# Performance work log

Hardware: AMD Instinct MI355X
Metric: run time of the kernel (lower is better)

Reference implementation:

```python
import jax, jax.numpy as jnp
import numpy as np

N_NODES = 100000


def gcn_conv(x, W, b, src, dst, n):
    # x: [N, Fin], W: [Fin, Fout]. GCNConv: D^-1/2 (A+I) D^-1/2 (X W) + b
    h = x @ W  # [N, Fout]
    ones = jnp.ones_like(dst, dtype=h.dtype)
    deg = jax.ops.segment_sum(ones, dst, num_segments=n)  # in-degree incl self-loops
    dinv = jnp.where(deg > 0, jax.lax.rsqrt(deg), 0.0)
    norm = dinv[src] * dinv[dst]  # [E]
    msg = h[src] * norm[:, None]  # gather + scale
    out = jax.ops.segment_sum(msg, dst, num_segments=n)  # scatter-add
    return out + b


def setup_inputs() -> dict:
    key = jax.random.key(0)
    k1, k2, k3, k4 = jax.random.split(key, 4)
    F_IN, H, C, E = 512, 256, 40, 3200000
    x = jax.random.normal(k1, (N_NODES, F_IN), dtype=jnp.float32)
    # glorot-ish init
    W1 = jax.random.normal(k2, (F_IN, H), dtype=jnp.float32) * (1.0 / np.sqrt(F_IN))
    b1 = jnp.zeros((H,), dtype=jnp.float32)
    W2 = jax.random.normal(k3, (H, C), dtype=jnp.float32) * (1.0 / np.sqrt(H))
    b2 = jnp.zeros((C,), dtype=jnp.float32)
    edge_index = jax.random.randint(k4, (2, E), 0, N_NODES, dtype=jnp.int64)
    return {"x": x, "W1": W1, "b1": b1, "W2": W2, "b2": b2, "edge_index": edge_index}


def reference(x, W1, b1, W2, b2, edge_index):
    n = x.shape[0]
    # add self-loops (PyG GCNConv default add_self_loops=True)
    loop = jnp.arange(n, dtype=edge_index.dtype)
    src = jnp.concatenate([edge_index[0], loop])
    dst = jnp.concatenate([edge_index[1], loop])
    h = gcn_conv(x, W1, b1, src, dst, n)
    h = jax.nn.relu(h)
    # F.dropout(training=self.training): identity in eval mode
    h = gcn_conv(h, W2, b2, src, dst, n)
    return jax.nn.log_softmax(h, axis=1)
```

## Files before the change

kernel.cpp:

```cpp
#include <hip/hip_runtime.h>
#include <stdint.h>

typedef __attribute__((ext_vector_type(8))) short bf16x8;
typedef __attribute__((ext_vector_type(4))) float f32x4;
typedef __attribute__((ext_vector_type(4))) int i32x4;
typedef __attribute__((ext_vector_type(2))) float f32x2;
typedef __attribute__((ext_vector_type(4))) unsigned int u32x4;
typedef __attribute__((ext_vector_type(8))) unsigned short ushort8_t;

__device__ __forceinline__ unsigned short f2bf(float f) {
    unsigned int u = __float_as_uint(f);
    u += 0x7FFFu + ((u >> 16) & 1u);
    return (unsigned short)(u >> 16);
}
__device__ __forceinline__ float bf2f(unsigned short s) {
    return __uint_as_float(((unsigned int)s) << 16);
}
__device__ __forceinline__ unsigned char fp8_enc(float f) {
    f = fminf(fmaxf(f, -448.f), 448.f);
    unsigned int u = __float_as_uint(f * 0x1p-120f);
    u += 0x7FFFFu + ((u >> 20) & 1u);
    return (unsigned char)(((u >> 20) & 0x7F) | ((u >> 24) & 0x80));
}

__device__ __forceinline__ f32x2 cvtpk0(unsigned int u) {
#if __has_builtin(__builtin_amdgcn_cvt_pk_f32_fp8)
    auto r = __builtin_amdgcn_cvt_pk_f32_fp8((int)u, false);
    f32x2 o; o.x = r[0]; o.y = r[1]; return o;
#else
    f32x2 o;
    o.x = __builtin_amdgcn_cvt_f32_fp8(u, 0);
    o.y = __builtin_amdgcn_cvt_f32_fp8(u, 1);
    return o;
#endif
}
__device__ __forceinline__ f32x2 cvtpk1(unsigned int u) {
#if __has_builtin(__builtin_amdgcn_cvt_pk_f32_fp8)
    auto r = __builtin_amdgcn_cvt_pk_f32_fp8((int)u, true);
    f32x2 o; o.x = r[0]; o.y = r[1]; return o;
#else
    f32x2 o;
    o.x = __builtin_amdgcn_cvt_f32_fp8(u, 2);
    o.y = __builtin_amdgcn_cvt_f32_fp8(u, 3);
    return o;
#endif
}

#define SLAB_CAP 5120

__global__ __launch_bounds__(256) void k_bscatter(const int* __restrict__ src,
                                                  const int* __restrict__ dst, int E,
                                                  int* __restrict__ bcnt,
                                                  int* __restrict__ slab, int nbuck) {
    __shared__ int lh[1024];
    __shared__ int lcur[1024];
    const int CH = 8192;
    int e0 = blockIdx.x * CH;
    int e1 = min(E, e0 + CH);
    for (int i = threadIdx.x; i < nbuck; i += 256) lh[i] = 0;
    __syncthreads();
    for (int i = e0 + threadIdx.x; i < e1; i += 256) atomicAdd(&lh[dst[i] >> 7], 1);
    __syncthreads();
    for (int i = threadIdx.x; i < nbuck; i += 256) {
        int c = lh[i];
        lh[i] = c ? atomicAdd(&bcnt[i], c) : 0;
        lcur[i] = 0;
    }
    __syncthreads();
    for (int i = e0 + threadIdx.x; i < e1; i += 256) {
        int d = dst[i], s = src[i];
        int b = d >> 7;
        int p = lh[b] + atomicAdd(&lcur[b], 1);
        if (p < SLAB_CAP) slab[(size_t)b * SLAB_CAP + p] = ((d & 127) << 20) | s;
    }
}

__global__ __launch_bounds__(1024) void k_bscan(const int* __restrict__ bcnt,
                                                int* __restrict__ bbase, int nbuck) {
    __shared__ int sh[1024];
    int t = threadIdx.x;
    int v = (t < nbuck) ? min(bcnt[t], SLAB_CAP) : 0;
    sh[t] = v;
    __syncthreads();
    for (int off = 1; off < 1024; off <<= 1) {
        int x = (t >= off) ? sh[t - off] : 0;
        __syncthreads();
        sh[t] += x;
        __syncthreads();
    }
    if (t < nbuck) bbase[t] = sh[t] - v;
    if (t == 1023) bbase[nbuck] = sh[1023];
}

__global__ __launch_bounds__(256) void k_bcsr(const int* __restrict__ slab,
                                              const int* __restrict__ bcnt,
                                              const int* __restrict__ bbase,
                                              int* __restrict__ rowp,
                                              int* __restrict__ col,
                                              float* __restrict__ dinv, int n, int nbuck) {
    __shared__ int lh[128], lsc[128], lcur[128];
    const int b = blockIdx.x;
    const int base = bbase[b];
    const int cnt = min(bcnt[b], SLAB_CAP);
    const int t = threadIdx.x;
    const int* sl = slab + (size_t)b * SLAB_CAP;
    if (t < 128) lh[t] = 0;
    __syncthreads();
    for (int i = t; i < cnt; i += 256) atomicAdd(&lh[sl[i] >> 20], 1);
    __syncthreads();
    if (t < 128) lsc[t] = lh[t];
    __syncthreads();
    for (int off = 1; off < 128; off <<= 1) {
        int x = (t < 128 && t >= off) ? lsc[t - off] : 0;
        __syncthreads();
        if (t < 128) lsc[t] += x;
        __syncthreads();
    }
    if (t < 128) {
        int excl = lsc[t] - lh[t];
        lcur[t] = excl;
        int v = (b << 7) + t;
        if (v < n) {
            rowp[v] = base + excl;
            dinv[v] = rsqrtf((float)lh[t] + 1.0f);
        }
    }
    if (b == 0 && t == 0) rowp[n] = bbase[nbuck];
    __syncthreads();
    for (int i = t; i < cnt; i += 256) {
        int pk = sl[i];
        int d = pk >> 20;
        int p = base + atomicAdd(&lcur[d], 1);
        col[p] = pk & 0xFFFFF;
    }
}

__global__ __launch_bounds__(256) void k_cvt_w(const float* __restrict__ W1,
                                               const float* __restrict__ W2,
                                               short* __restrict__ W1t,
                                               short* __restrict__ W2t,
                                               int n1, int n2) {
    int i = blockIdx.x * blockDim.x + threadIdx.x;
    if (i < n1) {
        int k = i >> 8, c = i & 255;
        W1t[(size_t)c * 512 + k] = (short)f2bf(W1[i]);
    } else if (i < n1 + n2) {
        int i2 = i - n1;
        int k = i2 / 40, c = i2 - k * 40;
        W2t[(size_t)c * 256 + k] = (short)f2bf(W2[i2]);
    }
}

__global__ __launch_bounds__(512) void k_gemm1(const float* __restrict__ A,
                                               const short* __restrict__ Bt,
                                               const float* __restrict__ dinv,
                                               unsigned char* __restrict__ outp, int M) {
    const int K = 512;
    __shared__ __align__(16) short As[128 * 32];
    __shared__ __align__(16) short Bs[256 * 32];
    const int tid = threadIdx.x;
    const int m0 = blockIdx.x * 128;
    const int w = tid >> 6, lane = tid & 63;
    const int quad = lane >> 4, l16 = lane & 15;
    const int mbase = (w >> 2) * 64, nbase = (w & 3) * 64;

    f32x4 acc[4][4];
#pragma unroll
    for (int i = 0; i < 4; i++)
#pragma unroll
        for (int j = 0; j < 4; j++) acc[i][j] = (f32x4){0.f, 0.f, 0.f, 0.f};

    for (int k0 = 0; k0 < K; k0 += 32) {
#pragma unroll
        for (int s = tid; s < 1024; s += 512) {
            int r = s >> 3, seg = s & 7;
            int gr = m0 + r;
            if (gr >= M) gr = M - 1;
            float4 v = *(const float4*)(A + (size_t)gr * K + k0 + seg * 4);
            ushort4 o;
            o.x = f2bf(v.x); o.y = f2bf(v.y); o.z = f2bf(v.z); o.w = f2bf(v.w);
            *(ushort4*)(As + r * 32 + seg * 4) = o;
        }
#pragma unroll
        for (int s = tid; s < 1024; s += 512) {
            int r = s >> 2, seg = s & 3;
            i32x4 v = *(const i32x4*)(Bt + (size_t)r * K + k0 + seg * 8);
            *(i32x4*)(Bs + r * 32 + seg * 8) = v;
        }
        __syncthreads();
        bf16x8 af[4], bfr[4];
#pragma unroll
        for (int i = 0; i < 4; i++)
            af[i] = *(const bf16x8*)(As + (mbase + i * 16 + l16) * 32 + quad * 8);
#pragma unroll
        for (int j = 0; j < 4; j++)
            bfr[j] = *(const bf16x8*)(Bs + (nbase + j * 16 + l16) * 32 + quad * 8);
#pragma unroll
        for (int i = 0; i < 4; i++)
#pragma unroll
            for (int j = 0; j < 4; j++)
                acc[i][j] = __builtin_amdgcn_mfma_f32_16x16x32_bf16(af[i], bfr[j], acc[i][j], 0, 0, 0);
        __syncthreads();
    }

#pragma unroll
    for (int i = 0; i < 4; i++) {
#pragma unroll
        for (int r = 0; r < 4; r++) {
            int row = m0 + mbase + i * 16 + quad * 4 + r;
            if (row < M) {
                float dv = dinv[row] * 64.f;
#pragma unroll
                for (int j = 0; j < 4; j++)
                    outp[(size_t)row * 256 + nbase + j * 16 + l16] =
                        fp8_enc(acc[i][j][r] * dv);
            }
        }
    }
}

__global__ __launch_bounds__(256) void k_gemm2(const short* __restrict__ A,
                                               const short* __restrict__ Bt,
                                               const float* __restrict__ dinv,
                                               unsigned char* __restrict__ outp, int M) {
    const int K = 256;
    __shared__ __align__(16) short As[128 * 32];
    __shared__ __align__(16) short Bs[64 * 32];
    const int tid = threadIdx.x;
    const int m0 = blockIdx.x * 128;
    const int w = tid >> 6, lane = tid & 63;
    const int quad = lane >> 4, l16 = lane & 15;
    const int mbase = (w >> 1) * 64, nbase = (w & 1) * 32;

    f32x4 acc[4][2];
#pragma unroll
    for (int i = 0; i < 4; i++)
#pragma unroll
        for (int j = 0; j < 2; j++) acc[i][j] = (f32x4){0.f, 0.f, 0.f, 0.f};

    for (int k0 = 0; k0 < K; k0 += 32) {
#pragma unroll
        for (int s = tid; s < 512; s += 256) {
            int r = s >> 2, seg = s & 3;
            int gr = m0 + r;
            if (gr >= M) gr = M - 1;
            i32x4 v = *(const i32x4*)(A + (size_t)gr * K + k0 + seg * 8);
            *(i32x4*)(As + r * 32 + seg * 8) = v;
        }
        if (tid < 256) {
            int r = tid >> 2, seg = tid & 3;
            i32x4 v = *(const i32x4*)(Bt + (size_t)r * K + k0 + seg * 8);
            *(i32x4*)(Bs + r * 32 + seg * 8) = v;
        }
        __syncthreads();
        bf16x8 af[4], bfr[2];
#pragma unroll
        for (int i = 0; i < 4; i++)
            af[i] = *(const bf16x8*)(As + (mbase + i * 16 + l16) * 32 + quad * 8);
#pragma unroll
        for (int j = 0; j < 2; j++)
            bfr[j] = *(const bf16x8*)(Bs + (nbase + j * 16 + l16) * 32 + quad * 8);
#pragma unroll
        for (int i = 0; i < 4; i++)
#pragma unroll
            for (int j = 0; j < 2; j++)
                acc[i][j] = __builtin_amdgcn_mfma_f32_16x16x32_bf16(af[i], bfr[j], acc[i][j], 0, 0, 0);
        __syncthreads();
    }

#pragma unroll
    for (int i = 0; i < 4; i++) {
#pragma unroll
        for (int r = 0; r < 4; r++) {
            int row = m0 + mbase + i * 16 + quad * 4 + r;
            if (row < M) {
                float dv = dinv[row] * 64.f;
#pragma unroll
                for (int j = 0; j < 2; j++)
                    outp[(size_t)row * 64 + nbase + j * 16 + l16] =
                        fp8_enc(acc[i][j][r] * dv);
            }
        }
    }
}

__global__ __launch_bounds__(256) void k_agg1(const unsigned char* __restrict__ h1p,
                                              const int* __restrict__ rowp,
                                              const int* __restrict__ col,
                                              const float* __restrict__ dinv,
                                              const float* __restrict__ b1,
                                              short* __restrict__ h2, int n) {
    const u32x4* __restrict__ hq = (const u32x4*)h1p;
    const int w = threadIdx.x >> 6, lane = threadIdx.x & 63;
    const int g = lane >> 4, sl = lane & 15;
    const int v = blockIdx.x * 4 + w;
    if (v >= n) return;

    f32x2 acc[8];
    {
        u32x4 q = (u32x4){0u, 0u, 0u, 0u};
        if (g == 0) q = hq[(size_t)v * 16 + sl];
#pragma unroll
        for (int i = 0; i < 4; i++) {
            acc[2 * i] = cvtpk0(q[i]);
            acc[2 * i + 1] = cvtpk1(q[i]);
        }
    }

    const int e0 = rowp[v], e1 = rowp[v + 1];
    const int nedge = e1 - e0;
    const int full = nedge & ~7;
    for (int t = 0; t < full; t += 8) {
        int ea = e0 + t + g;
        int sa = col[ea], sb = col[ea + 4];
        u32x4 qa = hq[(size_t)sa * 16 + sl];
        u32x4 qb = hq[(size_t)sb * 16 + sl];
#pragma unroll
        for (int i = 0; i < 4; i++) {
            acc[2 * i] += cvtpk0(qa[i]);
            acc[2 * i + 1] += cvtpk1(qa[i]);
        }
#pragma unroll
        for (int i = 0; i < 4; i++) {
            acc[2 * i] += cvtpk0(qb[i]);
            acc[2 * i + 1] += cvtpk1(qb[i]);
        }
    }
    for (int t = full + g; t < nedge; t += 4) {
        u32x4 q = hq[(size_t)col[e0 + t] * 16 + sl];
#pragma unroll
        for (int i = 0; i < 4; i++) {
            acc[2 * i] += cvtpk0(q[i]);
            acc[2 * i + 1] += cvtpk1(q[i]);
        }
    }

#pragma unroll
    for (int i = 0; i < 8; i++) {
        acc[i].x += __shfl_xor(acc[i].x, 16);
        acc[i].y += __shfl_xor(acc[i].y, 16);
        acc[i].x += __shfl_xor(acc[i].x, 32);
        acc[i].y += __shfl_xor(acc[i].y, 32);
    }

    if (g < 2) {
        const float dv = dinv[v] * 0x1p-6f;
        const float4* bq = (const float4*)(b1 + sl * 16 + g * 8);
        ushort8_t o;
#pragma unroll
        for (int k = 0; k < 2; k++) {
            float4 bb = bq[k];
            f32x2 p0 = acc[g * 4 + k * 2];
            f32x2 p1 = acc[g * 4 + k * 2 + 1];
            o[k * 4 + 0] = f2bf(fmaxf(fmaf(dv, p0.x, bb.x), 0.f));
            o[k * 4 + 1] = f2bf(fmaxf(fmaf(dv, p0.y, bb.y), 0.f));
            o[k * 4 + 2] = f2bf(fmaxf(fmaf(dv, p1.x, bb.z), 0.f));
            o[k * 4 + 3] = f2bf(fmaxf(fmaf(dv, p1.y, bb.w), 0.f));
        }
        *(ushort8_t*)(h2 + (size_t)v * 256 + sl * 16 + g * 8) = o;
    }
}

__global__ __launch_bounds__(256) void k_agg2(const unsigned char* __restrict__ zp,
                                              const int* __restrict__ rowp,
                                              const int* __restrict__ col,
                                              const float* __restrict__ dinv,
                                              const float* __restrict__ b2,
                                              float* __restrict__ out, int n) {
    const unsigned int* __restrict__ zw = (const unsigned int*)zp;
    const int w = threadIdx.x >> 6, lane = threadIdx.x & 63;
    const int g = lane >> 4, sl = lane & 15;
    const int v = blockIdx.x * 16 + w * 4 + g;
    if (v >= n) return;
    f32x2 a01, a23;
    {
        unsigned int u = zw[(size_t)v * 16 + sl];
        a01 = cvtpk0(u);
        a23 = cvtpk1(u);
    }
    const int e0 = rowp[v], e1 = rowp[v + 1];
    int e = e0;
    for (; e + 8 <= e1; e += 8) {
        int s0 = col[e], s1 = col[e + 1], s2 = col[e + 2], s3 = col[e + 3];
        int s4 = col[e + 4], s5 = col[e + 5], s6 = col[e + 6], s7 = col[e + 7];
        unsigned int u0 = zw[(size_t)s0 * 16 + sl];
        unsigned int u1 = zw[(size_t)s1 * 16 + sl];
        unsigned int u2 = zw[(size_t)s2 * 16 + sl];
        unsigned int u3 = zw[(size_t)s3 * 16 + sl];
        unsigned int u4 = zw[(size_t)s4 * 16 + sl];
        unsigned int u5 = zw[(size_t)s5 * 16 + sl];
        unsigned int u6 = zw[(size_t)s6 * 16 + sl];
        unsigned int u7 = zw[(size_t)s7 * 16 + sl];
        a01 += cvtpk0(u0) + cvtpk0(u1) + cvtpk0(u2) + cvtpk0(u3)
             + cvtpk0(u4) + cvtpk0(u5) + cvtpk0(u6) + cvtpk0(u7);
        a23 += cvtpk1(u0) + cvtpk1(u1) + cvtpk1(u2) + cvtpk1(u3)
             + cvtpk1(u4) + cvtpk1(u5) + cvtpk1(u6) + cvtpk1(u7);
    }
    for (; e + 2 <= e1; e += 2) {
        unsigned int u0 = zw[(size_t)col[e] * 16 + sl];
        unsigned int u1 = zw[(size_t)col[e + 1] * 16 + sl];
        a01 += cvtpk0(u0) + cvtpk0(u1);
        a23 += cvtpk1(u0) + cvtpk1(u1);
    }
    for (; e < e1; e++) {
        unsigned int u = zw[(size_t)col[e] * 16 + sl];
        a01 += cvtpk0(u);
        a23 += cvtpk1(u);
    }
    const int f = sl * 4;
    const float dv = dinv[v] * 0x1p-6f;
    float l0 = (f + 0 < 40) ? fmaf(dv, a01.x, b2[f + 0]) : -1e30f;
    float l1 = (f + 1 < 40) ? fmaf(dv, a01.y, b2[f + 1]) : -1e30f;
    float l2 = (f + 2 < 40) ? fmaf(dv, a23.x, b2[f + 2]) : -1e30f;
    float l3 = (f + 3 < 40) ? fmaf(dv, a23.y, b2[f + 3]) : -1e30f;
    float m = fmaxf(fmaxf(l0, l1), fmaxf(l2, l3));
    m = fmaxf(m, __shfl_xor(m, 1));
    m = fmaxf(m, __shfl_xor(m, 2));
    m = fmaxf(m, __shfl_xor(m, 4));
    m = fmaxf(m, __shfl_xor(m, 8));
    float es = expf(l0 - m) + expf(l1 - m) + expf(l2 - m) + expf(l3 - m);
    es += __shfl_xor(es, 1);
    es += __shfl_xor(es, 2);
    es += __shfl_xor(es, 4);
    es += __shfl_xor(es, 8);
    float ls = m + logf(es);
    if (sl < 10) {
        float4 o = {l0 - ls, l1 - ls, l2 - ls, l3 - ls};
        *(float4*)(out + (size_t)v * 40 + f) = o;
    }
}

extern "C" void kernel_launch(void* const* d_in, const int* in_sizes, int n_in,
                              void* d_out, int out_size, void* d_ws, size_t ws_size,
                              hipStream_t stream) {
    const float* x  = (const float*)d_in[0];
    const float* W1 = (const float*)d_in[1];
    const float* b1 = (const float*)d_in[2];
    const float* W2 = (const float*)d_in[3];
    const float* b2 = (const float*)d_in[4];
    const int*   ei = (const int*)d_in[5];
    float* out = (float*)d_out;

    const int FIN = 512, H = 256, C = 40;
    const int n = in_sizes[0] / FIN;
    const int E = in_sizes[5] / 2;
    const int nbuck = (n + 127) >> 7;

    auto align_up = [](size_t v) { return (v + 255) & ~(size_t)255; };
    char* base = (char*)d_ws;
    size_t off = 0;
    unsigned char* h1p = (unsigned char*)(base + off); off += align_up((size_t)n * H);
    short* h2    = (short*)(base + off); off += align_up((size_t)n * H * 2);
    unsigned char* zp = (unsigned char*)(base + off); off += align_up((size_t)n * 64);
    float* dinv  = (float*)(base + off); off += align_up((size_t)n * 4);
    int* rowp    = (int*)(base + off);   off += align_up((size_t)(n + 1) * 4);
    int* colarr  = (int*)(base + off);   off += align_up((size_t)E * 4);
    int* slab    = (int*)(base + off);   off += align_up((size_t)nbuck * SLAB_CAP * 4);
    short* W1t   = (short*)(base + off); off += align_up((size_t)H * FIN * 2);
    short* W2t   = (short*)(base + off); off += align_up((size_t)64 * H * 2);
    int* bcnt    = (int*)(base + off);   off += align_up((size_t)(nbuck + 1) * 4);
    int* bbase   = (int*)(base + off);   off += align_up((size_t)(nbuck + 1) * 4);

    const int* srcp = ei;
    const int* dstp = ei + E;

    hipMemsetAsync(bcnt, 0, (size_t)(nbuck + 1) * 4, stream);
    hipMemsetAsync(W2t, 0, (size_t)64 * H * 2, stream);

    k_bscatter<<<(E + 8191) / 8192, 256, 0, stream>>>(srcp, dstp, E, bcnt, slab, nbuck);
    k_bscan<<<1, 1024, 0, stream>>>(bcnt, bbase, nbuck);
    k_bcsr<<<nbuck, 256, 0, stream>>>(slab, bcnt, bbase, rowp, colarr, dinv, n, nbuck);

    int n1 = FIN * H, n2 = H * C;
    k_cvt_w<<<(n1 + n2 + 255) / 256, 256, 0, stream>>>(W1, W2, W1t, W2t, n1, n2);

    k_gemm1<<<(n + 127) / 128, 512, 0, stream>>>(x, W1t, dinv, h1p, n);
    k_agg1<<<(n + 3) / 4, 256, 0, stream>>>(h1p, rowp, colarr, dinv, b1, h2, n);

    k_gemm2<<<(n + 127) / 128, 256, 0, stream>>>(h2, W2t, dinv, zp, n);
    k_agg2<<<(n + 15) / 16, 256, 0, stream>>>(zp, rowp, colarr, dinv, b2, out, n);
}
```

Baseline: 632.8 us.

## Slice layer-1 fp8 features into 32-column planes and aggregate per slice

GEMM1 now writes its fp8 output as 8 column slices of 32 bytes per node instead of one 256-byte row. The first aggregation kernel is restructured so that each block handles a single slice for 128 nodes, with 8 lanes per node each gathering one 4-byte word per edge. The intent is to keep each slice's working set (about 3.2 MB) cache-resident so that random neighbour gathers hit L2/MALL more often. In exchange, the edge list and row pointers are read 8 times and each gather becomes a small 32-byte access.

```diff
diff --git a/kernel.cpp b/kernel.cpp
--- a/kernel.cpp
+++ b/kernel.cpp
@@ -5,8 +5,6 @@
 typedef __attribute__((ext_vector_type(4))) float f32x4;
 typedef __attribute__((ext_vector_type(4))) int i32x4;
 typedef __attribute__((ext_vector_type(2))) float f32x2;
-typedef __attribute__((ext_vector_type(4))) unsigned int u32x4;
-typedef __attribute__((ext_vector_type(8))) unsigned short ushort8_t;
 
 __device__ __forceinline__ unsigned short f2bf(float f) {
     unsigned int u = __float_as_uint(f);
@@ -203,6 +201,7 @@
         __syncthreads();
     }
 
+    const size_t slice_stride = (size_t)M * 32;
 #pragma unroll
     for (int i = 0; i < 4; i++) {
 #pragma unroll
@@ -211,9 +210,11 @@
             if (row < M) {
                 float dv = dinv[row] * 64.f;
 #pragma unroll
-                for (int j = 0; j < 4; j++)
-                    outp[(size_t)row * 256 + nbase + j * 16 + l16] =
+                for (int j = 0; j < 4; j++) {
+                    int c = nbase + j * 16 + l16;
+                    outp[(size_t)(c >> 5) * slice_stride + (size_t)row * 32 + (c & 31)] =
                         fp8_enc(acc[i][j][r] * dv);
+                }
             }
         }
     }
@@ -284,80 +285,54 @@
     }
 }
 
-__global__ __launch_bounds__(256) void k_agg1(const unsigned char* __restrict__ h1p,
+__global__ __launch_bounds__(256) void k_agg1(const unsigned char* __restrict__ h1s,
                                               const int* __restrict__ rowp,
                                               const int* __restrict__ col,
                                               const float* __restrict__ dinv,
                                               const float* __restrict__ b1,
                                               short* __restrict__ h2, int n) {
-    const u32x4* __restrict__ hq = (const u32x4*)h1p;
+    const int R = 4;
+    const int DPB = 4 * 8 * R;
+    const int slice = blockIdx.x & 7;
+    const int chunk = blockIdx.x >> 3;
     const int w = threadIdx.x >> 6, lane = threadIdx.x & 63;
-    const int g = lane >> 4, sl = lane & 15;
-    const int v = blockIdx.x * 4 + w;
-    if (v >= n) return;
-
-    f32x2 acc[8];
-    {
-        u32x4 q = (u32x4){0u, 0u, 0u, 0u};
-        if (g == 0) q = hq[(size_t)v * 16 + sl];
-#pragma unroll
-        for (int i = 0; i < 4; i++) {
-            acc[2 * i] = cvtpk0(q[i]);
-            acc[2 * i + 1] = cvtpk1(q[i]);
-        }
-    }
-
-    const int e0 = rowp[v], e1 = rowp[v + 1];
-    const int nedge = e1 - e0;
-    const int full = nedge & ~7;
-    for (int t = 0; t < full; t += 8) {
-        int ea = e0 + t + g;
-        int sa = col[ea], sb = col[ea + 4];
-        u32x4 qa = hq[(size_t)sa * 16 + sl];
-        u32x4 qb = hq[(size_t)sb * 16 + sl];
-#pragma unroll
-        for (int i = 0; i < 4; i++) {
-            acc[2 * i] += cvtpk0(qa[i]);
-            acc[2 * i + 1] += cvtpk1(qa[i]);
-        }
-#pragma unroll
-        for (int i = 0; i < 4; i++) {
-            acc[2 * i] += cvtpk0(qb[i]);
-            acc[2 * i + 1] += cvtpk1(qb[i]);
-        }
-    }
-    for (int t = full + g; t < nedge; t += 4) {
-        u32x4 q = hq[(size_t)col[e0 + t] * 16 + sl];
-#pragma unroll
-        for (int i = 0; i < 4; i++) {
-            acc[2 * i] += cvtpk0(q[i]);
-            acc[2 * i + 1] += cvtpk1(q[i]);
-        }
-    }
-
-#pragma unroll
-    for (int i = 0; i < 8; i++) {
-        acc[i].x += __shfl_xor(acc[i].x, 16);
-        acc[i].y += __shfl_xor(acc[i].y, 16);
-        acc[i].x += __shfl_xor(acc[i].x, 32);
-        acc[i].y += __shfl_xor(acc[i].y, 32);
-    }
-
-    if (g < 2) {
-        const float dv = dinv[v] * 0x1p-6f;
-        const float4* bq = (const float4*)(b1 + sl * 16 + g * 8);
-        ushort8_t o;
-#pragma unroll
-        for (int k = 0; k < 2; k++) {
-            float4 bb = bq[k];
-            f32x2 p0 = acc[g * 4 + k * 2];
-            f32x2 p1 = acc[g * 4 + k * 2 + 1];
-            o[k * 4 + 0] = f2bf(fmaxf(fmaf(dv, p0.x, bb.x), 0.f));
-            o[k * 4 + 1] = f2bf(fmaxf(fmaf(dv, p0.y, bb.y), 0.f));
-            o[k * 4 + 2] = f2bf(fmaxf(fmaf(dv, p1.x, bb.z), 0.f));
-            o[k * 4 + 3] = f2bf(fmaxf(fmaf(dv, p1.y, bb.w), 0.f));
-        }
-        *(ushort8_t*)(h2 + (size_t)v * 256 + sl * 16 + g * 8) = o;
+    const int g = lane >> 3, sl = lane & 7;
+    const unsigned int* __restrict__ hw =
+        (const unsigned int*)(h1s + (size_t)slice * ((size_t)n * 32));
+    const int f0 = slice * 32 + sl * 4;
+    const float4 bb = *(const float4*)(b1 + f0);
+    const int vbase = chunk * DPB + w * (8 * R);
+
+    for (int r = 0; r < R; r++) {
+        const int v = vbase + r * 8 + g;
+        const int vc = min(v, n - 1);
+        const int e0 = rowp[vc], e1 = rowp[vc + 1];
+        unsigned int u = hw[(size_t)vc * 8 + sl];
+        f32x2 a0 = cvtpk0(u), a1 = cvtpk1(u);
+        int e = e0;
+        for (; e + 4 <= e1; e += 4) {
+            int s0 = col[e], s1 = col[e + 1], s2 = col[e + 2], s3 = col[e + 3];
+            unsigned int q0 = hw[(size_t)s0 * 8 + sl];
+            unsigned int q1 = hw[(size_t)s1 * 8 + sl];
+            unsigned int q2 = hw[(size_t)s2 * 8 + sl];
+            unsigned int q3 = hw[(size_t)s3 * 8 + sl];
+            a0 += cvtpk0(q0) + cvtpk0(q1) + cvtpk0(q2) + cvtpk0(q3);
+            a1 += cvtpk1(q0) + cvtpk1(q1) + cvtpk1(q2) + cvtpk1(q3);
+        }
+        for (; e < e1; e++) {
+            unsigned int q = hw[(size_t)col[e] * 8 + sl];
+            a0 += cvtpk0(q);
+            a1 += cvtpk1(q);
+        }
+        if (v < n) {
+            const float d = dinv[vc] * 0x1p-6f;
+            ushort4 o;
+            o.x = f2bf(fmaxf(fmaf(d, a0.x, bb.x), 0.f));
+            o.y = f2bf(fmaxf(fmaf(d, a0.y, bb.y), 0.f));
+            o.z = f2bf(fmaxf(fmaf(d, a1.x, bb.z), 0.f));
+            o.w = f2bf(fmaxf(fmaf(d, a1.y, bb.w), 0.f));
+            *(ushort4*)(h2 + (size_t)v * 256 + f0) = o;
+        }
     }
 }
 
@@ -475,7 +450,7 @@
     k_cvt_w<<<(n1 + n2 + 255) / 256, 256, 0, stream>>>(W1, W2, W1t, W2t, n1, n2);
 
     k_gemm1<<<(n + 127) / 128, 512, 0, stream>>>(x, W1t, dinv, h1p, n);
-    k_agg1<<<(n + 3) / 4, 256, 0, stream>>>(h1p, rowp, colarr, dinv, b1, h2, n);
+    k_agg1<<<8 * ((n + 127) / 128), 256, 0, stream>>>(h1p, rowp, colarr, dinv, b1, h2, n);
 
     k_gemm2<<<(n + 127) / 128, 256, 0, stream>>>(h2, W2t, dinv, zp, n);
     k_agg2<<<(n + 15) / 16, 256, 0, stream>>>(zp, rowp, colarr, dinv, b2, out, n);
```

Result: slower. 699.8 us (+10.6%).
